# Kernel tuning notes

Hardware: AMD Instinct MI355X
Metric: run time of the kernel (lower is better)

Reference implementation:

```python
import jax, jax.numpy as jnp
import numpy as np

B, L, D = 8, 512, 128

def setup_inputs() -> dict:
    key = jax.random.key(0)
    k1, k2, k3, k4 = jax.random.split(key, 4)
    inp = jax.random.normal(k1, (B, L, D), dtype=jnp.float32)
    # torch.nn.Linear weights: y = x @ W.T, scaled small for stability
    u_w = jax.random.normal(k2, (D, D), dtype=jnp.float32) / np.sqrt(D)
    v_w = jax.random.normal(k3, (D, D), dtype=jnp.float32) / np.sqrt(D)
    a_w = jax.random.normal(k4, (1, D), dtype=jnp.float32) / np.sqrt(D)
    return {"inp": inp, "u_w": u_w, "v_w": v_w, "a_w": a_w}

def reference(inp, u_w, v_w, a_w):
    # mlp attention: score[b,i,j] = a( tanh( u(inp)[b,j] + v(inp)[b,i] ) )
    q = jnp.einsum('bld,ed->ble', inp, u_w)   # u(inp), [B,L,D]
    k = jnp.einsum('bld,ed->ble', inp, v_w)   # v(inp), [B,L,D]
    # query expanded over axis 1 (i), key over axis 2 (j): score[b,i,j,:] = q[b,j] + k[b,i]
    s = jnp.tanh(q[:, None, :, :] + k[:, :, None, :])      # [B,L,L,D] -- the big intermediate
    score = jnp.einsum('bijd,d->bij', s, a_w[0])            # [B,L,L]
    attn = jax.nn.softmax(score, axis=2)
    out = jnp.einsum('bij,bjd->bid', attn, inp)             # [B,L,D]
    return out, attn
```

## Files before the change

### kernel.cpp

```cpp
#include <hip/hip_runtime.h>

#define NB 8
#define NL 512
#define ND 128

constexpr float CEXP = 2.8853900817779268f;

typedef float v2f __attribute__((ext_vector_type(2)));

__global__ __launch_bounds__(256) void wpack_kernel(
    const float* __restrict__ uw, const float* __restrict__ vw,
    float* __restrict__ uwp, float* __restrict__ vwp) {
  const int m = blockIdx.x >> 4;
  const int t = (blockIdx.x & 15) * 256 + threadIdx.x;
  const float4* src = (const float4*)(m ? vw : uw);
  float4* dst = (float4*)(m ? vwp : uwp);
  const int e = t >> 5, d4 = t & 31;
  float4 v = src[e * 32 + d4];
  dst[d4 * 128 + e] = v;
}

__global__ __launch_bounds__(256) void qk_kernel(
    const float* __restrict__ inp, const float* __restrict__ uwp,
    const float* __restrict__ vwp, float* __restrict__ eqp,
    float* __restrict__ ekq) {
  __shared__ float qt[128][9];
  const int b = blockIdx.x & 7;
  const int l0 = (blockIdx.x >> 3) * 8;
  const int tid = threadIdx.x;

  const int e = tid & 127;
  const int half = tid >> 7;
  const float* xrow = inp + (b * NL + l0) * ND;
  const float4* W4 = (const float4*)(half ? vwp : uwp) + e;
  float acc[8];
#pragma unroll
  for (int r = 0; r < 8; ++r) acc[r] = 0.f;
  float4 w = W4[0];
  for (int d4 = 0; d4 < 32; ++d4) {
    float4 wn = W4[(size_t)((d4 + 1 > 31) ? 31 : d4 + 1) * 128];
#pragma unroll
    for (int r = 0; r < 8; ++r) {
      float4 x = *((const float4*)&xrow[r * ND + 4 * d4]);
      acc[r] = fmaf(w.x, x.x, acc[r]);
      acc[r] = fmaf(w.y, x.y, acc[r]);
      acc[r] = fmaf(w.z, x.z, acc[r]);
      acc[r] = fmaf(w.w, x.w, acc[r]);
    }
    w = wn;
  }
  if (half) {
    float* ekb = ekq + ((size_t)(b * 64 + (l0 >> 3)) * 128 + e) * 8;
#pragma unroll
    for (int r = 0; r < 8; ++r) {
      const int slot = (r & 3) * 2 + (r >> 2);
      ekb[slot] = __builtin_amdgcn_exp2f(CEXP * acc[r]);
    }
  } else {
#pragma unroll
    for (int r = 0; r < 8; ++r)
      qt[e][r] = __builtin_amdgcn_exp2f(CEXP * acc[r]);
  }
  __syncthreads();
  if (!half) {
  }
  {
    const int e4 = tid >> 3, r = tid & 7;
    float4 v = make_float4(qt[4 * e4][r], qt[4 * e4 + 1][r],
                           qt[4 * e4 + 2][r], qt[4 * e4 + 3][r]);
    ((float4*)eqp)[(b * 32 + e4) * NL + l0 + r] = v;
  }
}

__global__ __launch_bounds__(512, 4) void attn_kernel(
    const float* __restrict__ inp, const float* __restrict__ aw,
    const float* __restrict__ eqp, const float* __restrict__ ekq,
    float* __restrict__ out, float* __restrict__ attn) {
  __shared__ v2f red[8][8][64];
  __shared__ float attn_lds[8][512];
  __shared__ float rsum[8][8];

  const int b = blockIdx.x & 7;
  const int i0 = (blockIdx.x >> 3) * 8;
  const int tid = threadIdx.x;
  const int lane = tid & 63;
  const int wid = tid >> 6;

  v2f acc04 = {0.f, 0.f}, acc15 = {0.f, 0.f};
  v2f acc26 = {0.f, 0.f}, acc37 = {0.f, 0.f};
  const v2f ONE2 = {1.f, 1.f};
  const float4* eq4 = (const float4*)eqp + (size_t)(b * 32) * NL + tid;
  const float4* aw4 = (const float4*)aw;
  const v2f* ekq2 =
      (const v2f*)(ekq + (size_t)(b * 64 + (i0 >> 3)) * 128 * 8);
  float4 eA = eq4[0];
  float4 eB = eq4[NL];
#pragma unroll 4
  for (int d4 = 0; d4 < 32; ++d4) {
    const int nf = (d4 + 2 > 31) ? 31 : d4 + 2;
    float4 eC = eq4[(size_t)nf * NL];
    float4 na4 = aw4[d4];
#pragma unroll
    for (int dd = 0; dd < 4; ++dd) {
      const int d = 4 * d4 + dd;
      const float eqs = (dd == 0) ? eA.x : (dd == 1) ? eA.y
                       : (dd == 2) ? eA.z : eA.w;
      const float na = (dd == 0) ? na4.x : (dd == 1) ? na4.y
                      : (dd == 2) ? na4.z : na4.w;
      v2f e01 = ekq2[d * 4 + 0];
      v2f e23 = ekq2[d * 4 + 1];
      v2f e45 = ekq2[d * 4 + 2];
      v2f e67 = ekq2[d * 4 + 3];
      v2f eq2 = {eqs, eqs};
      v2f Pa = __builtin_elementwise_fma(eq2, e01, ONE2);
      v2f Pb = __builtin_elementwise_fma(eq2, e23, ONE2);
      v2f Pc = __builtin_elementwise_fma(eq2, e45, ONE2);
      v2f Pd = __builtin_elementwise_fma(eq2, e67, ONE2);
      v2f M1 = Pa * Pb;
      v2f M2 = Pc * Pd;
      v2f Q = M1 * M2;
      v2f NR = {na * __builtin_amdgcn_rcpf(Q.x),
                na * __builtin_amdgcn_rcpf(Q.y)};
      v2f T = NR * M2;
      v2f U = NR * M1;
      acc04 = __builtin_elementwise_fma(T, Pb, acc04);
      acc15 = __builtin_elementwise_fma(T, Pa, acc15);
      acc26 = __builtin_elementwise_fma(U, Pd, acc26);
      acc37 = __builtin_elementwise_fma(U, Pc, acc37);
    }
    eA = eB;
    eB = eC;
  }
  float acc[8] = {acc04.x, acc15.x, acc26.x, acc37.x,
                  acc04.y, acc15.y, acc26.y, acc37.y};

  float sinv[8], ex[8];
#pragma unroll
  for (int i = 0; i < 8; ++i) {
    float e = __builtin_amdgcn_exp2f(acc[i] * (-CEXP));
    ex[i] = e;
    float s = e;
#pragma unroll
    for (int off = 32; off; off >>= 1) s += __shfl_xor(s, off);
    if (lane == 0) rsum[wid][i] = s;
  }
  __syncthreads();
#pragma unroll
  for (int i = 0; i < 8; ++i) {
    float s = ((rsum[0][i] + rsum[1][i]) + (rsum[2][i] + rsum[3][i])) +
              ((rsum[4][i] + rsum[5][i]) + (rsum[6][i] + rsum[7][i]));
    sinv[i] = __builtin_amdgcn_rcpf(s);
  }

  float* attnb = attn + (size_t)(b * NL + i0) * NL;
#pragma unroll
  for (int i = 0; i < 8; ++i) {
    float a = ex[i] * sinv[i];
    attn_lds[i][tid] = a;
    attnb[i * NL + tid] = a;
  }
  __syncthreads();

  v2f po[8];
#pragma unroll
  for (int i = 0; i < 8; ++i) po[i] = (v2f){0.f, 0.f};
  const v2f* inp2 = (const v2f*)(inp + b * NL * ND);
  for (int jj4 = 0; jj4 < 16; ++jj4) {
    const int jc = wid * 64 + jj4 * 4;
    v2f x0 = inp2[(jc + 0) * 64 + lane];
    v2f x1 = inp2[(jc + 1) * 64 + lane];
    v2f x2 = inp2[(jc + 2) * 64 + lane];
    v2f x3 = inp2[(jc + 3) * 64 + lane];
#pragma unroll
    for (int i = 0; i < 8; ++i) {
      float4 a4 = *((const float4*)&attn_lds[i][jc]);
      po[i] = __builtin_elementwise_fma((v2f){a4.x, a4.x}, x0, po[i]);
      po[i] = __builtin_elementwise_fma((v2f){a4.y, a4.y}, x1, po[i]);
      po[i] = __builtin_elementwise_fma((v2f){a4.z, a4.z}, x2, po[i]);
      po[i] = __builtin_elementwise_fma((v2f){a4.w, a4.w}, x3, po[i]);
    }
  }
#pragma unroll
  for (int i = 0; i < 8; ++i) red[wid][i][lane] = po[i];
  __syncthreads();
  {
    const int i2 = wid, dl = lane;
    v2f s = red[0][i2][dl];
#pragma unroll
    for (int p = 1; p < 8; ++p) s += red[p][i2][dl];
    *(v2f*)&out[(size_t)(b * NL + i0 + i2) * ND + dl * 2] = s;
  }
}

extern "C" void kernel_launch(void* const* d_in, const int* in_sizes, int n_in,
                              void* d_out, int out_size, void* d_ws,
                              size_t ws_size, hipStream_t stream) {
  const float* inp = (const float*)d_in[0];
  const float* uw = (const float*)d_in[1];
  const float* vw = (const float*)d_in[2];
  const float* aw = (const float*)d_in[3];
  float* out = (float*)d_out;
  float* attn = out + NB * NL * ND;
  float* eqp = (float*)d_ws;
  float* ekq = eqp + NB * ND * NL;
  size_t need = (size_t)2 * NB * ND * NL * 4 + 32768 * 4;
  float* wp = (ws_size >= need) ? (ekq + NB * ND * NL) : (attn);
  float* uwp = wp;
  float* vwp = wp + 16384;
  wpack_kernel<<<dim3(32), 256, 0, stream>>>(uw, vw, uwp, vwp);
  qk_kernel<<<dim3(NB * 64), 256, 0, stream>>>(inp, uwp, vwp, eqp, ekq);
  attn_kernel<<<dim3(NB * 64), 512, 0, stream>>>(inp, aw, eqp, ekq, out, attn);
}
```

Baseline: 53.82 us.

## Split attention score feature dimension across two thread halves with 1024-thread blocks

The attention kernel now launches 1024 threads per block. Each half of the block computes partial scores over half of the 128 feature dimensions, and the partials are combined through shared memory before the softmax. The output matmul is split so each wave handles 4 rows instead of 8. The aim is more parallelism and latency hiding in the dominant score loop, at the cost of an extra reduction barrier, idle threads during the softmax, and register pressure from __launch_bounds__(1024, 8).

Result: slower. 75.99 us (+41.2%).

```diff
diff --git a/kernel.cpp b/kernel.cpp
--- a/kernel.cpp
+++ b/kernel.cpp
@@ -62,8 +62,6 @@
       qt[e][r] = __builtin_amdgcn_exp2f(CEXP * acc[r]);
   }
   __syncthreads();
-  if (!half) {
-  }
   {
     const int e4 = tid >> 3, r = tid & 7;
     float4 v = make_float4(qt[4 * e4][r], qt[4 * e4 + 1][r],
@@ -72,7 +70,7 @@
   }
 }
 
-__global__ __launch_bounds__(512, 4) void attn_kernel(
+__global__ __launch_bounds__(1024, 8) void attn_kernel(
     const float* __restrict__ inp, const float* __restrict__ aw,
     const float* __restrict__ eqp, const float* __restrict__ ekq,
     float* __restrict__ out, float* __restrict__ attn) {
@@ -85,19 +83,22 @@
   const int tid = threadIdx.x;
   const int lane = tid & 63;
   const int wid = tid >> 6;
+  const int j = tid & 511;
+  const int dh = tid >> 9;
 
   v2f acc04 = {0.f, 0.f}, acc15 = {0.f, 0.f};
   v2f acc26 = {0.f, 0.f}, acc37 = {0.f, 0.f};
   const v2f ONE2 = {1.f, 1.f};
-  const float4* eq4 = (const float4*)eqp + (size_t)(b * 32) * NL + tid;
-  const float4* aw4 = (const float4*)aw;
+  const float4* eq4 =
+      (const float4*)eqp + (size_t)(b * 32 + dh * 16) * NL + j;
+  const float4* aw4 = (const float4*)aw + dh * 16;
   const v2f* ekq2 =
-      (const v2f*)(ekq + (size_t)(b * 64 + (i0 >> 3)) * 128 * 8);
+      (const v2f*)(ekq + (size_t)(b * 64 + (i0 >> 3)) * 128 * 8) + dh * 256;
   float4 eA = eq4[0];
   float4 eB = eq4[NL];
 #pragma unroll 4
-  for (int d4 = 0; d4 < 32; ++d4) {
-    const int nf = (d4 + 2 > 31) ? 31 : d4 + 2;
+  for (int d4 = 0; d4 < 16; ++d4) {
+    const int nf = (d4 + 2 > 15) ? 15 : d4 + 2;
     float4 eC = eq4[(size_t)nf * NL];
     float4 na4 = aw4[d4];
 #pragma unroll
@@ -134,46 +135,55 @@
   float acc[8] = {acc04.x, acc15.x, acc26.x, acc37.x,
                   acc04.y, acc15.y, acc26.y, acc37.y};
 
-  float sinv[8], ex[8];
-#pragma unroll
-  for (int i = 0; i < 8; ++i) {
-    float e = __builtin_amdgcn_exp2f(acc[i] * (-CEXP));
-    ex[i] = e;
-    float s = e;
-#pragma unroll
-    for (int off = 32; off; off >>= 1) s += __shfl_xor(s, off);
-    if (lane == 0) rsum[wid][i] = s;
-  }
-  __syncthreads();
-#pragma unroll
-  for (int i = 0; i < 8; ++i) {
-    float s = ((rsum[0][i] + rsum[1][i]) + (rsum[2][i] + rsum[3][i])) +
-              ((rsum[4][i] + rsum[5][i]) + (rsum[6][i] + rsum[7][i]));
-    sinv[i] = __builtin_amdgcn_rcpf(s);
-  }
-
-  float* attnb = attn + (size_t)(b * NL + i0) * NL;
-#pragma unroll
-  for (int i = 0; i < 8; ++i) {
-    float a = ex[i] * sinv[i];
-    attn_lds[i][tid] = a;
-    attnb[i * NL + tid] = a;
-  }
-  __syncthreads();
-
-  v2f po[8];
-#pragma unroll
-  for (int i = 0; i < 8; ++i) po[i] = (v2f){0.f, 0.f};
+  float* accred = (float*)red;
+  if (dh) {
+#pragma unroll
+    for (int i = 0; i < 8; ++i) accred[i * 512 + j] = acc[i];
+  }
+  __syncthreads();
+
+  float ex[8];
+  if (!dh) {
+#pragma unroll
+    for (int i = 0; i < 8; ++i) {
+      float a = acc[i] + accred[i * 512 + j];
+      float e = __builtin_amdgcn_exp2f(a * (-CEXP));
+      ex[i] = e;
+      float s = e;
+#pragma unroll
+      for (int off = 32; off; off >>= 1) s += __shfl_xor(s, off);
+      if (lane == 0) rsum[wid][i] = s;
+    }
+  }
+  __syncthreads();
+  if (!dh) {
+    float* attnb = attn + (size_t)(b * NL + i0) * NL;
+#pragma unroll
+    for (int i = 0; i < 8; ++i) {
+      float s = ((rsum[0][i] + rsum[1][i]) + (rsum[2][i] + rsum[3][i])) +
+                ((rsum[4][i] + rsum[5][i]) + (rsum[6][i] + rsum[7][i]));
+      float a = ex[i] * __builtin_amdgcn_rcpf(s);
+      attn_lds[i][j] = a;
+      attnb[i * NL + j] = a;
+    }
+  }
+  __syncthreads();
+
+  const int jbase = (wid & 7) * 64;
+  const int rg = wid >> 3;
+  v2f po[4];
+#pragma unroll
+  for (int i = 0; i < 4; ++i) po[i] = (v2f){0.f, 0.f};
   const v2f* inp2 = (const v2f*)(inp + b * NL * ND);
   for (int jj4 = 0; jj4 < 16; ++jj4) {
-    const int jc = wid * 64 + jj4 * 4;
+    const int jc = jbase + jj4 * 4;
     v2f x0 = inp2[(jc + 0) * 64 + lane];
     v2f x1 = inp2[(jc + 1) * 64 + lane];
     v2f x2 = inp2[(jc + 2) * 64 + lane];
     v2f x3 = inp2[(jc + 3) * 64 + lane];
 #pragma unroll
-    for (int i = 0; i < 8; ++i) {
-      float4 a4 = *((const float4*)&attn_lds[i][jc]);
+    for (int i = 0; i < 4; ++i) {
+      float4 a4 = *((const float4*)&attn_lds[rg * 4 + i][jc]);
       po[i] = __builtin_elementwise_fma((v2f){a4.x, a4.x}, x0, po[i]);
       po[i] = __builtin_elementwise_fma((v2f){a4.y, a4.y}, x1, po[i]);
       po[i] = __builtin_elementwise_fma((v2f){a4.z, a4.z}, x2, po[i]);
@@ -181,9 +191,9 @@
     }
   }
 #pragma unroll
-  for (int i = 0; i < 8; ++i) red[wid][i][lane] = po[i];
-  __syncthreads();
-  {
+  for (int i = 0; i < 4; ++i) red[wid & 7][rg * 4 + i][lane] = po[i];
+  __syncthreads();
+  if (wid < 8) {
     const int i2 = wid, dl = lane;
     v2f s = red[0][i2][dl];
 #pragma unroll
@@ -209,5 +219,5 @@
   float* vwp = wp + 16384;
   wpack_kernel<<<dim3(32), 256, 0, stream>>>(uw, vw, uwp, vwp);
   qk_kernel<<<dim3(NB * 64), 256, 0, stream>>>(inp, uwp, vwp, eqp, ekq);
-  attn_kernel<<<dim3(NB * 64), 512, 0, stream>>>(inp, aw, eqp, ekq, out, attn);
-}
+  attn_kernel<<<dim3(NB * 64), 1024, 0, stream>>>(inp, aw, eqp, ekq, out, attn);
+}
```

## Halve rows per attention block to double grid and raise occupancy

Applied to the files above, without the earlier changes.

The attention kernel now processes 4 query rows per block instead of 8, launching twice as many blocks with an 8-blocks-per-CU launch bound. The key-exponential buffer is re-laid out in 4-row groups and written with float4 stores to match. This aims to fill the GPU better and increase latency hiding, but it doubles reloads of the query-exponential stream per output row and amortises each reciprocal over fewer rows.

Result: slower. 57.62 us (+7.1%).

```diff
diff --git a/kernel.cpp b/kernel.cpp
--- a/kernel.cpp
+++ b/kernel.cpp
@@ -50,20 +50,21 @@
     w = wn;
   }
   if (half) {
-    float* ekb = ekq + ((size_t)(b * 64 + (l0 >> 3)) * 128 + e) * 8;
-#pragma unroll
-    for (int r = 0; r < 8; ++r) {
-      const int slot = (r & 3) * 2 + (r >> 2);
-      ekb[slot] = __builtin_amdgcn_exp2f(CEXP * acc[r]);
-    }
+    float ek[8];
+#pragma unroll
+    for (int r = 0; r < 8; ++r)
+      ek[r] = __builtin_amdgcn_exp2f(CEXP * acc[r]);
+    float4 lo = make_float4(ek[0], ek[2], ek[1], ek[3]);
+    float4 hi = make_float4(ek[4], ek[6], ek[5], ek[7]);
+    float4* ekb = (float4*)ekq + (size_t)(b * 128 + (l0 >> 2)) * 128 + e;
+    ekb[0] = lo;
+    ekb[128] = hi;
   } else {
 #pragma unroll
     for (int r = 0; r < 8; ++r)
       qt[e][r] = __builtin_amdgcn_exp2f(CEXP * acc[r]);
   }
   __syncthreads();
-  if (!half) {
-  }
   {
     const int e4 = tid >> 3, r = tid & 7;
     float4 v = make_float4(qt[4 * e4][r], qt[4 * e4 + 1][r],
@@ -72,27 +73,26 @@
   }
 }
 
-__global__ __launch_bounds__(512, 4) void attn_kernel(
+__global__ __launch_bounds__(512, 8) void attn_kernel(
     const float* __restrict__ inp, const float* __restrict__ aw,
     const float* __restrict__ eqp, const float* __restrict__ ekq,
     float* __restrict__ out, float* __restrict__ attn) {
-  __shared__ v2f red[8][8][64];
-  __shared__ float attn_lds[8][512];
-  __shared__ float rsum[8][8];
+  __shared__ v2f red[8][4][64];
+  __shared__ float attn_lds[4][512];
+  __shared__ float rsum[8][4];
 
   const int b = blockIdx.x & 7;
-  const int i0 = (blockIdx.x >> 3) * 8;
+  const int i0 = (blockIdx.x >> 3) * 4;
   const int tid = threadIdx.x;
   const int lane = tid & 63;
   const int wid = tid >> 6;
 
-  v2f acc04 = {0.f, 0.f}, acc15 = {0.f, 0.f};
-  v2f acc26 = {0.f, 0.f}, acc37 = {0.f, 0.f};
+  v2f acc02 = {0.f, 0.f}, acc13 = {0.f, 0.f};
   const v2f ONE2 = {1.f, 1.f};
   const float4* eq4 = (const float4*)eqp + (size_t)(b * 32) * NL + tid;
   const float4* aw4 = (const float4*)aw;
   const v2f* ekq2 =
-      (const v2f*)(ekq + (size_t)(b * 64 + (i0 >> 3)) * 128 * 8);
+      (const v2f*)(ekq + (size_t)(b * 128 + (i0 >> 2)) * 128 * 4);
   float4 eA = eq4[0];
   float4 eB = eq4[NL];
 #pragma unroll 4
@@ -107,36 +107,25 @@
                        : (dd == 2) ? eA.z : eA.w;
       const float na = (dd == 0) ? na4.x : (dd == 1) ? na4.y
                       : (dd == 2) ? na4.z : na4.w;
-      v2f e01 = ekq2[d * 4 + 0];
-      v2f e23 = ekq2[d * 4 + 1];
-      v2f e45 = ekq2[d * 4 + 2];
-      v2f e67 = ekq2[d * 4 + 3];
+      v2f e02 = ekq2[d * 2 + 0];
+      v2f e13 = ekq2[d * 2 + 1];
       v2f eq2 = {eqs, eqs};
-      v2f Pa = __builtin_elementwise_fma(eq2, e01, ONE2);
-      v2f Pb = __builtin_elementwise_fma(eq2, e23, ONE2);
-      v2f Pc = __builtin_elementwise_fma(eq2, e45, ONE2);
-      v2f Pd = __builtin_elementwise_fma(eq2, e67, ONE2);
-      v2f M1 = Pa * Pb;
-      v2f M2 = Pc * Pd;
-      v2f Q = M1 * M2;
-      v2f NR = {na * __builtin_amdgcn_rcpf(Q.x),
-                na * __builtin_amdgcn_rcpf(Q.y)};
-      v2f T = NR * M2;
-      v2f U = NR * M1;
-      acc04 = __builtin_elementwise_fma(T, Pb, acc04);
-      acc15 = __builtin_elementwise_fma(T, Pa, acc15);
-      acc26 = __builtin_elementwise_fma(U, Pd, acc26);
-      acc37 = __builtin_elementwise_fma(U, Pc, acc37);
+      v2f Pa = __builtin_elementwise_fma(eq2, e02, ONE2);
+      v2f Pb = __builtin_elementwise_fma(eq2, e13, ONE2);
+      v2f M = Pa * Pb;
+      v2f NR = {na * __builtin_amdgcn_rcpf(M.x),
+                na * __builtin_amdgcn_rcpf(M.y)};
+      acc02 = __builtin_elementwise_fma(NR, Pb, acc02);
+      acc13 = __builtin_elementwise_fma(NR, Pa, acc13);
     }
     eA = eB;
     eB = eC;
   }
-  float acc[8] = {acc04.x, acc15.x, acc26.x, acc37.x,
-                  acc04.y, acc15.y, acc26.y, acc37.y};
-
-  float sinv[8], ex[8];
-#pragma unroll
-  for (int i = 0; i < 8; ++i) {
+  float acc[4] = {acc02.x, acc13.x, acc02.y, acc13.y};
+
+  float sinv[4], ex[4];
+#pragma unroll
+  for (int i = 0; i < 4; ++i) {
     float e = __builtin_amdgcn_exp2f(acc[i] * (-CEXP));
     ex[i] = e;
     float s = e;
@@ -146,7 +135,7 @@
   }
   __syncthreads();
 #pragma unroll
-  for (int i = 0; i < 8; ++i) {
+  for (int i = 0; i < 4; ++i) {
     float s = ((rsum[0][i] + rsum[1][i]) + (rsum[2][i] + rsum[3][i])) +
               ((rsum[4][i] + rsum[5][i]) + (rsum[6][i] + rsum[7][i]));
     sinv[i] = __builtin_amdgcn_rcpf(s);
@@ -154,16 +143,16 @@
 
   float* attnb = attn + (size_t)(b * NL + i0) * NL;
 #pragma unroll
-  for (int i = 0; i < 8; ++i) {
+  for (int i = 0; i < 4; ++i) {
     float a = ex[i] * sinv[i];
     attn_lds[i][tid] = a;
     attnb[i * NL + tid] = a;
   }
   __syncthreads();
 
-  v2f po[8];
-#pragma unroll
-  for (int i = 0; i < 8; ++i) po[i] = (v2f){0.f, 0.f};
+  v2f po[4];
+#pragma unroll
+  for (int i = 0; i < 4; ++i) po[i] = (v2f){0.f, 0.f};
   const v2f* inp2 = (const v2f*)(inp + b * NL * ND);
   for (int jj4 = 0; jj4 < 16; ++jj4) {
     const int jc = wid * 64 + jj4 * 4;
@@ -172,7 +161,7 @@
     v2f x2 = inp2[(jc + 2) * 64 + lane];
     v2f x3 = inp2[(jc + 3) * 64 + lane];
 #pragma unroll
-    for (int i = 0; i < 8; ++i) {
+    for (int i = 0; i < 4; ++i) {
       float4 a4 = *((const float4*)&attn_lds[i][jc]);
       po[i] = __builtin_elementwise_fma((v2f){a4.x, a4.x}, x0, po[i]);
       po[i] = __builtin_elementwise_fma((v2f){a4.y, a4.y}, x1, po[i]);
@@ -181,9 +170,9 @@
     }
   }
 #pragma unroll
-  for (int i = 0; i < 8; ++i) red[wid][i][lane] = po[i];
-  __syncthreads();
-  {
+  for (int i = 0; i < 4; ++i) red[wid][i][lane] = po[i];
+  __syncthreads();
+  if (wid < 4) {
     const int i2 = wid, dl = lane;
     v2f s = red[0][i2][dl];
 #pragma unroll
@@ -209,5 +198,5 @@
   float* vwp = wp + 16384;
   wpack_kernel<<<dim3(32), 256, 0, stream>>>(uw, vw, uwp, vwp);
   qk_kernel<<<dim3(NB * 64), 256, 0, stream>>>(inp, uwp, vwp, eqp, ekq);
-  attn_kernel<<<dim3(NB * 64), 512, 0, stream>>>(inp, aw, eqp, ekq, out, attn);
-}
+  attn_kernel<<<dim3(NB * 128), 512, 0, stream>>>(inp, aw, eqp, ekq, out, attn);
+}
```

## Process 16 query rows per attention block to reuse eq loads

Applied to the files above, without the earlier changes.

Each attention block now handles 16 rows instead of 8, halving the grid to 256 blocks. The ek layout in qk_kernel is regrouped into 16-row tiles written with float4 stores. Each eq value and each inp row loaded from global memory is now reused across twice as many rows. In exchange, register pressure and LDS use rise, and the smaller grid (256 blocks on a large GPU) may leave compute units underused.

Result: slower. 57.32 us (+6.5%).

```diff
diff --git a/kernel.cpp b/kernel.cpp
--- a/kernel.cpp
+++ b/kernel.cpp
@@ -50,20 +50,22 @@
     w = wn;
   }
   if (half) {
-    float* ekb = ekq + ((size_t)(b * 64 + (l0 >> 3)) * 128 + e) * 8;
-#pragma unroll
-    for (int r = 0; r < 8; ++r) {
-      const int slot = (r & 3) * 2 + (r >> 2);
-      ekb[slot] = __builtin_amdgcn_exp2f(CEXP * acc[r]);
-    }
+    float ek[8];
+#pragma unroll
+    for (int r = 0; r < 8; ++r)
+      ek[r] = __builtin_amdgcn_exp2f(CEXP * acc[r]);
+    float4 lo = make_float4(ek[0], ek[4], ek[1], ek[5]);
+    float4 hi = make_float4(ek[2], ek[6], ek[3], ek[7]);
+    float* ekb = ekq + ((size_t)(b * 32 + (l0 >> 4)) * 128 + e) * 16 +
+                 ((l0 >> 3) & 1) * 8;
+    *(float4*)&ekb[0] = lo;
+    *(float4*)&ekb[4] = hi;
   } else {
 #pragma unroll
     for (int r = 0; r < 8; ++r)
       qt[e][r] = __builtin_amdgcn_exp2f(CEXP * acc[r]);
   }
   __syncthreads();
-  if (!half) {
-  }
   {
     const int e4 = tid >> 3, r = tid & 7;
     float4 v = make_float4(qt[4 * e4][r], qt[4 * e4 + 1][r],
@@ -77,22 +79,24 @@
     const float* __restrict__ eqp, const float* __restrict__ ekq,
     float* __restrict__ out, float* __restrict__ attn) {
   __shared__ v2f red[8][8][64];
-  __shared__ float attn_lds[8][512];
-  __shared__ float rsum[8][8];
+  __shared__ float attn_lds[16][512];
+  __shared__ float rsum[8][16];
 
   const int b = blockIdx.x & 7;
-  const int i0 = (blockIdx.x >> 3) * 8;
+  const int i0 = (blockIdx.x >> 3) * 16;
   const int tid = threadIdx.x;
   const int lane = tid & 63;
   const int wid = tid >> 6;
 
   v2f acc04 = {0.f, 0.f}, acc15 = {0.f, 0.f};
   v2f acc26 = {0.f, 0.f}, acc37 = {0.f, 0.f};
+  v2f acc8C = {0.f, 0.f}, acc9D = {0.f, 0.f};
+  v2f accAE = {0.f, 0.f}, accBF = {0.f, 0.f};
   const v2f ONE2 = {1.f, 1.f};
   const float4* eq4 = (const float4*)eqp + (size_t)(b * 32) * NL + tid;
   const float4* aw4 = (const float4*)aw;
   const v2f* ekq2 =
-      (const v2f*)(ekq + (size_t)(b * 64 + (i0 >> 3)) * 128 * 8);
+      (const v2f*)(ekq + (size_t)(b * 32 + (i0 >> 4)) * 128 * 16);
   float4 eA = eq4[0];
   float4 eB = eq4[NL];
 #pragma unroll 4
@@ -107,36 +111,62 @@
                        : (dd == 2) ? eA.z : eA.w;
       const float na = (dd == 0) ? na4.x : (dd == 1) ? na4.y
                       : (dd == 2) ? na4.z : na4.w;
-      v2f e01 = ekq2[d * 4 + 0];
-      v2f e23 = ekq2[d * 4 + 1];
-      v2f e45 = ekq2[d * 4 + 2];
-      v2f e67 = ekq2[d * 4 + 3];
       v2f eq2 = {eqs, eqs};
-      v2f Pa = __builtin_elementwise_fma(eq2, e01, ONE2);
-      v2f Pb = __builtin_elementwise_fma(eq2, e23, ONE2);
-      v2f Pc = __builtin_elementwise_fma(eq2, e45, ONE2);
-      v2f Pd = __builtin_elementwise_fma(eq2, e67, ONE2);
-      v2f M1 = Pa * Pb;
-      v2f M2 = Pc * Pd;
-      v2f Q = M1 * M2;
-      v2f NR = {na * __builtin_amdgcn_rcpf(Q.x),
-                na * __builtin_amdgcn_rcpf(Q.y)};
-      v2f T = NR * M2;
-      v2f U = NR * M1;
-      acc04 = __builtin_elementwise_fma(T, Pb, acc04);
-      acc15 = __builtin_elementwise_fma(T, Pa, acc15);
-      acc26 = __builtin_elementwise_fma(U, Pd, acc26);
-      acc37 = __builtin_elementwise_fma(U, Pc, acc37);
+      v2f NA2 = {na, na};
+      {
+        v2f e01 = ekq2[d * 8 + 0];
+        v2f e23 = ekq2[d * 8 + 1];
+        v2f e45 = ekq2[d * 8 + 2];
+        v2f e67 = ekq2[d * 8 + 3];
+        v2f Pa = __builtin_elementwise_fma(eq2, e01, ONE2);
+        v2f Pb = __builtin_elementwise_fma(eq2, e23, ONE2);
+        v2f Pc = __builtin_elementwise_fma(eq2, e45, ONE2);
+        v2f Pd = __builtin_elementwise_fma(eq2, e67, ONE2);
+        v2f M1 = Pa * Pb;
+        v2f M2 = Pc * Pd;
+        v2f Q = M1 * M2;
+        v2f R = {__builtin_amdgcn_rcpf(Q.x), __builtin_amdgcn_rcpf(Q.y)};
+        v2f NR = NA2 * R;
+        v2f T = NR * M2;
+        v2f U = NR * M1;
+        acc04 = __builtin_elementwise_fma(T, Pb, acc04);
+        acc15 = __builtin_elementwise_fma(T, Pa, acc15);
+        acc26 = __builtin_elementwise_fma(U, Pd, acc26);
+        acc37 = __builtin_elementwise_fma(U, Pc, acc37);
+      }
+      {
+        v2f e01 = ekq2[d * 8 + 4];
+        v2f e23 = ekq2[d * 8 + 5];
+        v2f e45 = ekq2[d * 8 + 6];
+        v2f e67 = ekq2[d * 8 + 7];
+        v2f Pa = __builtin_elementwise_fma(eq2, e01, ONE2);
+        v2f Pb = __builtin_elementwise_fma(eq2, e23, ONE2);
+        v2f Pc = __builtin_elementwise_fma(eq2, e45, ONE2);
+        v2f Pd = __builtin_elementwise_fma(eq2, e67, ONE2);
+        v2f M1 = Pa * Pb;
+        v2f M2 = Pc * Pd;
+        v2f Q = M1 * M2;
+        v2f R = {__builtin_amdgcn_rcpf(Q.x), __builtin_amdgcn_rcpf(Q.y)};
+        v2f NR = NA2 * R;
+        v2f T = NR * M2;
+        v2f U = NR * M1;
+        acc8C = __builtin_elementwise_fma(T, Pb, acc8C);
+        acc9D = __builtin_elementwise_fma(T, Pa, acc9D);
+        accAE = __builtin_elementwise_fma(U, Pd, accAE);
+        accBF = __builtin_elementwise_fma(U, Pc, accBF);
+      }
     }
     eA = eB;
     eB = eC;
   }
-  float acc[8] = {acc04.x, acc15.x, acc26.x, acc37.x,
-                  acc04.y, acc15.y, acc26.y, acc37.y};
-
-  float sinv[8], ex[8];
-#pragma unroll
-  for (int i = 0; i < 8; ++i) {
+  float acc[16] = {acc04.x, acc15.x, acc26.x, acc37.x,
+                   acc04.y, acc15.y, acc26.y, acc37.y,
+                   acc8C.x, acc9D.x, accAE.x, accBF.x,
+                   acc8C.y, acc9D.y, accAE.y, accBF.y};
+
+  float ex[16];
+#pragma unroll
+  for (int i = 0; i < 16; ++i) {
     float e = __builtin_amdgcn_exp2f(acc[i] * (-CEXP));
     ex[i] = e;
     float s = e;
@@ -145,25 +175,20 @@
     if (lane == 0) rsum[wid][i] = s;
   }
   __syncthreads();
-#pragma unroll
-  for (int i = 0; i < 8; ++i) {
+  float* attnb = attn + (size_t)(b * NL + i0) * NL;
+#pragma unroll
+  for (int i = 0; i < 16; ++i) {
     float s = ((rsum[0][i] + rsum[1][i]) + (rsum[2][i] + rsum[3][i])) +
               ((rsum[4][i] + rsum[5][i]) + (rsum[6][i] + rsum[7][i]));
-    sinv[i] = __builtin_amdgcn_rcpf(s);
-  }
-
-  float* attnb = attn + (size_t)(b * NL + i0) * NL;
-#pragma unroll
-  for (int i = 0; i < 8; ++i) {
-    float a = ex[i] * sinv[i];
+    float a = ex[i] * __builtin_amdgcn_rcpf(s);
     attn_lds[i][tid] = a;
     attnb[i * NL + tid] = a;
   }
   __syncthreads();
 
-  v2f po[8];
-#pragma unroll
-  for (int i = 0; i < 8; ++i) po[i] = (v2f){0.f, 0.f};
+  v2f po[16];
+#pragma unroll
+  for (int i = 0; i < 16; ++i) po[i] = (v2f){0.f, 0.f};
   const v2f* inp2 = (const v2f*)(inp + b * NL * ND);
   for (int jj4 = 0; jj4 < 16; ++jj4) {
     const int jc = wid * 64 + jj4 * 4;
@@ -172,7 +197,7 @@
     v2f x2 = inp2[(jc + 2) * 64 + lane];
     v2f x3 = inp2[(jc + 3) * 64 + lane];
 #pragma unroll
-    for (int i = 0; i < 8; ++i) {
+    for (int i = 0; i < 16; ++i) {
       float4 a4 = *((const float4*)&attn_lds[i][jc]);
       po[i] = __builtin_elementwise_fma((v2f){a4.x, a4.x}, x0, po[i]);
       po[i] = __builtin_elementwise_fma((v2f){a4.y, a4.y}, x1, po[i]);
@@ -181,14 +206,18 @@
     }
   }
 #pragma unroll
-  for (int i = 0; i < 8; ++i) red[wid][i][lane] = po[i];
-  __syncthreads();
-  {
-    const int i2 = wid, dl = lane;
-    v2f s = red[0][i2][dl];
-#pragma unroll
-    for (int p = 1; p < 8; ++p) s += red[p][i2][dl];
-    *(v2f*)&out[(size_t)(b * NL + i0 + i2) * ND + dl * 2] = s;
+  for (int h = 0; h < 2; ++h) {
+#pragma unroll
+    for (int i = 0; i < 8; ++i) red[wid][i][lane] = po[h * 8 + i];
+    __syncthreads();
+    {
+      const int i2 = wid, dl = lane;
+      v2f s = red[0][i2][dl];
+#pragma unroll
+      for (int p = 1; p < 8; ++p) s += red[p][i2][dl];
+      *(v2f*)&out[(size_t)(b * NL + i0 + h * 8 + i2) * ND + dl * 2] = s;
+    }
+    if (h == 0) __syncthreads();
   }
 }
 
@@ -209,5 +238,5 @@
   float* vwp = wp + 16384;
   wpack_kernel<<<dim3(32), 256, 0, stream>>>(uw, vw, uwp, vwp);
   qk_kernel<<<dim3(NB * 64), 256, 0, stream>>>(inp, uwp, vwp, eqp, ekq);
-  attn_kernel<<<dim3(NB * 64), 512, 0, stream>>>(inp, aw, eqp, ekq, out, attn);
-}
+  attn_kernel<<<dim3(NB * 32), 512, 0, stream>>>(inp, aw, eqp, ekq, out, attn);
+}
```
